# Optimization experiments

Measured on AMD Instinct MI355X. Metric: run time of the kernel, lower is better.

## Reference

```python
import jax, jax.numpy as jnp
import numpy as np

EMB = 256
N_NODES = 100000
N_EDGES = 500000
N_REL = 10
REL_DIM = 64
HID = 128
HEADS = 4
HEAD_DIM = HID // HEADS


def setup_inputs() -> dict:
    key = jax.random.key(0)
    ks = jax.random.split(key, 16)
    s = lambda i, shape: jax.random.normal(ks[i], shape, dtype=jnp.float32) * 0.05
    return {
        "node_embeddings": jax.random.normal(ks[0], (N_NODES, EMB), dtype=jnp.float32),
        "edge_index": jax.random.randint(ks[1], (2, N_EDGES), 0, N_NODES),
        "relation_type": jax.random.randint(ks[2], (N_EDGES,), 0, N_REL),
        "rel_emb": s(3, (N_REL, REL_DIM)),
        "W_edge": s(4, (2 * EMB, HID)), "b_edge": jnp.zeros((HID,), jnp.float32),
        "W_q": s(5, (REL_DIM, HID)), "b_q": jnp.zeros((HID,), jnp.float32),
        "W_k": s(6, (HID, HID)), "b_k": jnp.zeros((HID,), jnp.float32),
        "W_v": s(7, (HID, HID)), "b_v": jnp.zeros((HID,), jnp.float32),
        "W_o1": s(8, (HID, HID)), "b_o1": jnp.zeros((HID,), jnp.float32),
        "W_o2": s(9, (HID, 1)), "b_o2": jnp.zeros((1,), jnp.float32),
    }


def reference(node_embeddings, edge_index, relation_type, rel_emb,
              W_edge, b_edge, W_q, b_q, W_k, b_k, W_v, b_v,
              W_o1, b_o1, W_o2, b_o2):
    # Gather endpoint features: [E, 2*EMB]
    src = node_embeddings[edge_index[0]]
    tgt = node_embeddings[edge_index[1]]
    edge_features = jnp.concatenate([src, tgt], axis=1)
    # Edge MLP (dropout is identity at eval): [E, HID]
    edge_hidden = jax.nn.relu(edge_features @ W_edge + b_edge)
    # Relation embedding lookup: [E, REL_DIM]
    rel = rel_emb[relation_type]
    E = edge_hidden.shape[0]
    Q = (rel @ W_q + b_q).reshape(E, HEADS, HEAD_DIM)
    K = (edge_hidden @ W_k + b_k).reshape(E, HEADS, HEAD_DIM)
    V = (edge_hidden @ W_v + b_v).reshape(E, HEADS, HEAD_DIM)
    scale = jnp.sqrt(jnp.float32(HEAD_DIM))
    scores = jnp.sum(Q * K, axis=-1) / scale          # [E, HEADS]
    attn = jax.nn.softmax(scores, axis=-1)            # softmax over heads
    attended = (attn[..., None] * V).reshape(E, HID)
    output = attended + edge_hidden
    # Output MLP: Linear->ReLU->Linear(1)
    h = jax.nn.relu(output @ W_o1 + b_o1)
    score = (h @ W_o2 + b_o2).squeeze(-1)             # [E]
    return score
```

## Files before the change

### kernel.cpp

```cpp
#include <hip/hip_runtime.h>

#define EMB   256
#define HID   128
#define RELD  64
#define NREL  10
#define TE    128

typedef __attribute__((ext_vector_type(8)))  short bf16x8;
typedef __attribute__((ext_vector_type(16))) float f32x16;

__device__ __forceinline__ float bf16_to_f32(unsigned short u) {
    union { unsigned int i; float f; } v;
    v.i = ((unsigned int)u) << 16;
    return v.f;
}

__device__ __forceinline__ unsigned short f32_to_bf16(float x) {
    union { unsigned int i; float f; } v;
    v.f = x;
    unsigned int b = v.i;
    unsigned int rounded = b + 0x7fffu + ((b >> 16) & 1u);
    return (unsigned short)(rounded >> 16);
}

template <bool F32>
__device__ __forceinline__ float ldx(const void* p, size_t i) {
    if (F32) return ((const float*)p)[i];
    return bf16_to_f32(((const unsigned short*)p)[i]);
}

__device__ __forceinline__ bool detect_f32(const void* nodeEmb) {
    const float* f = (const float*)nodeEmb;
    float x = f[(threadIdx.x & 63) * 997];
    bool sane = isfinite(x) && fabsf(x) < 1.0e6f;
    unsigned long long m = __ballot(sane);
    return __popcll(m) >= 48;
}

__device__ __forceinline__ void gload16(const void* g, void* l) {
    __builtin_amdgcn_global_load_lds(
        (const __attribute__((address_space(1))) unsigned int*)g,
        (__attribute__((address_space(3))) unsigned int*)l, 16, 0, 0);
}

template <bool F32>
__device__ void prep_body(int vb, const void* W_edge, const void* W_k,
                          const void* W_v, const void* W_o1, const void* rel_emb,
                          const void* W_q, const void* b_q,
                          unsigned short* WTe, unsigned short* WTk,
                          unsigned short* WTv, unsigned short* WTo1, float* Qtab)
{
    if (vb < 448) {
        int idx = vb * 256 + threadIdx.x;
        if (idx < 65536) {
            int kc = idx >> 12, e = idx & 4095;
            int g = e >> 3, j = e & 7;
            int col = g & 127, kg = g >> 7;
            int k = kc * 32 + kg * 8 + j;
            WTe[idx] = f32_to_bf16(ldx<F32>(W_edge, (size_t)k * HID + col));
        } else if (idx < 65536 + 16384) {
            int i = idx - 65536;
            int kc = i >> 12, e = i & 4095;
            int g = e >> 3, j = e & 7;
            int col = g & 127, kg = (g >> 7) & 3;
            int k = kc * 32 + kg * 8 + j;
            WTk[i] = f32_to_bf16(ldx<F32>(W_k, (size_t)k * HID + col));
        } else if (idx < 65536 + 2 * 16384) {
            int i = idx - 65536 - 16384;
            int kc = i >> 12, e = i & 4095;
            int g = e >> 3, j = e & 7;
            int col = g & 127, kg = (g >> 7) & 3;
            int k = kc * 32 + kg * 8 + j;
            WTv[i] = f32_to_bf16(ldx<F32>(W_v, (size_t)k * HID + col));
        } else {
            int i = idx - 65536 - 2 * 16384;
            int kc = i >> 12, e = i & 4095;
            int g = e >> 3, j = e & 7;
            int col = g & 127, kg = (g >> 7) & 3;
            int k = kc * 32 + kg * 8 + j;
            WTo1[i] = f32_to_bf16(ldx<F32>(W_o1, (size_t)k * HID + col));
        }
    } else {
        const int t = threadIdx.x;
        const int c = t & (HID - 1);
        const int h = t >> 7;
        for (int r = h; r < NREL; r += 2) {
            float acc = 0.f;
            for (int d = 0; d < RELD; ++d)
                acc += ldx<F32>(rel_emb, r * RELD + d) * ldx<F32>(W_q, (size_t)d * HID + c);
            Qtab[r * HID + c] = acc + ldx<F32>(b_q, c);
        }
    }
}

__global__ void prep_kernel(const void* nodeEmb,
                            const void* W_edge, const void* W_k, const void* W_v,
                            const void* W_o1, const void* rel_emb, const void* W_q,
                            const void* b_q,
                            unsigned short* WTe, unsigned short* WTk,
                            unsigned short* WTv, unsigned short* WTo1, float* Qtab,
                            unsigned short* nodeBf16, int convBlocks,
                            unsigned long long nodeElems)
{
    bool f32 = detect_f32(nodeEmb);
    int b = blockIdx.x;
    if (b < convBlocks) {
        if (!f32) return;
        unsigned long long i = (unsigned long long)b * 2048ull + threadIdx.x * 8;
        if (i + 8 <= nodeElems) {
            const float* src = (const float*)nodeEmb + i;
            float4 f0 = *(const float4*)src;
            float4 f1 = *(const float4*)(src + 4);
            union { unsigned short us[8]; uint4 v; } pk;
            pk.us[0] = f32_to_bf16(f0.x); pk.us[1] = f32_to_bf16(f0.y);
            pk.us[2] = f32_to_bf16(f0.z); pk.us[3] = f32_to_bf16(f0.w);
            pk.us[4] = f32_to_bf16(f1.x); pk.us[5] = f32_to_bf16(f1.y);
            pk.us[6] = f32_to_bf16(f1.z); pk.us[7] = f32_to_bf16(f1.w);
            *(uint4*)(nodeBf16 + i) = pk.v;
        }
        return;
    }
    b -= convBlocks;
    if (f32) prep_body<true >(b, W_edge, W_k, W_v, W_o1, rel_emb, W_q, b_q,
                              WTe, WTk, WTv, WTo1, Qtab);
    else     prep_body<false>(b, W_edge, W_k, W_v, W_o1, rel_emb, W_q, b_q,
                              WTe, WTk, WTv, WTo1, Qtab);
}

struct __align__(16) Smem {
    unsigned short sHid[16 * 128 * 8];
    unsigned short SA[2][4096];
    unsigned short SB[2][4096];
    float sQf[NREL * HID];
    float sBias[5 * HID];
    float sSc[TE][4];
    float sAttn[TE][4];
    float sPart[TE][2];
    int   sSrc[TE], sTgt[TE], sRel[TE];
};

__device__ __forceinline__ int shid_idx(int row, int k) {
    return (((k >> 3) * 128 + row) << 3) + (k & 7);
}

template <bool F32, bool GBF16>
__device__ void fused_body(
    Smem& sm,
    const void* gsrc, const int* edgeIdx, const int* relType,
    const unsigned short* WTe, const unsigned short* WTk,
    const unsigned short* WTv, const unsigned short* WTo1,
    const void* b_edge, const void* b_k, const void* b_v,
    const void* b_o1, const void* W_o2, const void* b_o2,
    const float* Qtab, void* outp, int E)
{
    const int t   = threadIdx.x;
    const int l   = t & 63;
    const int w   = t >> 6;
    const int c   = l & 31;
    const int h5  = l >> 5;
    const int rt  = w >> 1;
    const int cg2 = w & 1;
    const int bs  = blockIdx.x * TE;
    const int aRow = 32 * rt + c;

    if (t < TE) {
        int e = bs + t;
        if (e >= E) e = E - 1;
        if (e < 0)  e = 0;
        sm.sSrc[t] = edgeIdx[e];
        sm.sTgt[t] = edgeIdx[E + e];
        int r = relType[e];
        if (r < 0) r = 0;
        if (r >= NREL) r = NREL - 1;
        sm.sRel[t] = r;
    }
    for (int i = t; i < 5 * HID; i += 512) {
        int which = i >> 7, j = i & (HID - 1);
        float v = (which == 0) ? ldx<F32>(b_edge, j)
                : (which == 1) ? ldx<F32>(b_k, j)
                : (which == 2) ? ldx<F32>(b_v, j)
                : (which == 3) ? ldx<F32>(b_o1, j)
                               : ldx<F32>(W_o2, j);
        sm.sBias[i] = v;
    }
    for (int i = t; i < NREL * HID; i += 512)
        sm.sQf[i] = Qtab[i];
    __syncthreads();

    const int    stS   = t >> 8;
    const int    stH5  = (t >> 7) & 1;
    const int    stRow = t & 127;
    const size_t rowOffS = (size_t)sm.sSrc[stRow] * EMB;
    const size_t rowOffT = (size_t)sm.sTgt[stRow] * EMB;
    const int    colSub  = stS * 16 + stH5 * 8;
    char* const  ldsWaveA0 = (char*)sm.SA[0] + w * 1024;
    char* const  ldsWaveA1 = (char*)sm.SA[1] + w * 1024;
    char* const  ldsWaveB0 = (char*)sm.SB[0] + w * 1024;
    char* const  ldsWaveB1 = (char*)sm.SB[1] + w * 1024;

    #define STAGE_A(kc, buf)                                                     \
    {                                                                            \
        size_t eoff = (((kc) < 8) ? rowOffS : rowOffT)                           \
                      + (size_t)(((kc) & 7) * 32 + colSub);                      \
        if (GBF16) {                                                             \
            gload16((const unsigned short*)gsrc + eoff,                          \
                    (buf) ? ldsWaveA1 : ldsWaveA0);                              \
        } else {                                                                 \
            const float* p_ = (const float*)gsrc + eoff;                         \
            float4 f0_ = *(const float4*)p_;                                     \
            float4 f1_ = *(const float4*)(p_ + 4);                               \
            union { unsigned short us[8]; uint4 v; } pk_;                        \
            pk_.us[0] = f32_to_bf16(f0_.x); pk_.us[1] = f32_to_bf16(f0_.y);      \
            pk_.us[2] = f32_to_bf16(f0_.z); pk_.us[3] = f32_to_bf16(f0_.w);      \
            pk_.us[4] = f32_to_bf16(f1_.x); pk_.us[5] = f32_to_bf16(f1_.y);      \
            pk_.us[6] = f32_to_bf16(f1_.z); pk_.us[7] = f32_to_bf16(f1_.w);      \
            *(uint4*)((char*)sm.SA[(buf)] + t * 16) = pk_.v;                     \
        }                                                                        \
    }

    #define STAGE_B(WT, kc, buf)                                                 \
        gload16((WT) + (kc) * 4096 + t * 8, (buf) ? ldsWaveB1 : ldsWaveB0);

    #define MFMA_SA(buf, accv)                                                   \
    {                                                                            \
        const char* sa_ = (const char*)sm.SA[(buf)];                             \
        const char* sb_ = (const char*)sm.SB[(buf)];                             \
        _Pragma("unroll")                                                        \
        for (int s_ = 0; s_ < 2; ++s_) {                                         \
            bf16x8 a_ = *(const bf16x8*)(sa_ + ((s_ * 256 + h5 * 128 + aRow) << 4)); \
            _Pragma("unroll")                                                    \
            for (int ct_ = 0; ct_ < 2; ++ct_) {                                  \
                bf16x8 b_ = *(const bf16x8*)                                     \
                    (sb_ + ((s_ * 256 + h5 * 128 + 64 * cg2 + 32 * ct_ + c) << 4)); \
                accv[ct_] = __builtin_amdgcn_mfma_f32_32x32x16_bf16(             \
                                a_, b_, accv[ct_], 0, 0, 0);                     \
            }                                                                    \
        }                                                                        \
    }

    #define MFMA_H(kc, buf, accv)                                                \
    {                                                                            \
        const char* sb_ = (const char*)sm.SB[(buf)];                             \
        _Pragma("unroll")                                                        \
        for (int s_ = 0; s_ < 2; ++s_) {                                         \
            bf16x8 a_ = *(const bf16x8*)((const char*)sm.sHid +                  \
                         ((((kc) * 4 + s_ * 2 + h5) * 128 + aRow) << 4));        \
            _Pragma("unroll")                                                    \
            for (int ct_ = 0; ct_ < 2; ++ct_) {                                  \
                bf16x8 b_ = *(const bf16x8*)                                     \
                    (sb_ + ((s_ * 256 + h5 * 128 + 64 * cg2 + 32 * ct_ + c) << 4)); \
                accv[ct_] = __builtin_amdgcn_mfma_f32_32x32x16_bf16(             \
                                a_, b_, accv[ct_], 0, 0, 0);                     \
            }                                                                    \
        }                                                                        \
    }

    f32x16 acc[2];
    acc[0] = (f32x16)(0.0f); acc[1] = (f32x16)(0.0f);
    STAGE_A(0, 0); STAGE_B(WTe, 0, 0);
    __syncthreads();
    #pragma unroll
    for (int kc = 0; kc < 16; ++kc) {
        int buf = kc & 1;
        if (kc < 15) { STAGE_A(kc + 1, buf ^ 1); STAGE_B(WTe, kc + 1, buf ^ 1); }
        MFMA_SA(buf, acc);
        __syncthreads();
    }
    {
        #pragma unroll
        for (int ct = 0; ct < 2; ++ct) {
            int col = 64 * cg2 + 32 * ct + c;
            float bb = sm.sBias[col];
            #pragma unroll
            for (int r = 0; r < 16; ++r) {
                int erow = 32 * rt + (r & 3) + 8 * (r >> 2) + 4 * h5;
                sm.sHid[shid_idx(erow, col)] = f32_to_bf16(fmaxf(acc[ct][r] + bb, 0.f));
            }
        }
    }

    f32x16 kacc[2];
    kacc[0] = (f32x16)(0.0f); kacc[1] = (f32x16)(0.0f);
    STAGE_B(WTk, 0, 0);
    __syncthreads();
    #pragma unroll
    for (int kc = 0; kc < 4; ++kc) {
        int buf = kc & 1;
        if (kc < 3) STAGE_B(WTk, kc + 1, buf ^ 1);
        MFMA_H(kc, buf, kacc);
        __syncthreads();
    }

    {
        float ps[2][16];
        #pragma unroll
        for (int ct = 0; ct < 2; ++ct) {
            int col = 64 * cg2 + 32 * ct + c;
            float bk = sm.sBias[HID + col];
            #pragma unroll
            for (int r = 0; r < 16; ++r) {
                int erow = 32 * rt + (r & 3) + 8 * (r >> 2) + 4 * h5;
                ps[ct][r] = (kacc[ct][r] + bk) * sm.sQf[sm.sRel[erow] * HID + col];
            }
        }
        #pragma unroll
        for (int m = 1; m < 32; m <<= 1)
            #pragma unroll
            for (int ct = 0; ct < 2; ++ct)
                #pragma unroll
                for (int r = 0; r < 16; ++r)
                    ps[ct][r] += __shfl_xor(ps[ct][r], m, 64);
        if (c == 0) {
            const float inv = 0.17677669529663687f;
            #pragma unroll
            for (int ct = 0; ct < 2; ++ct) {
                int head = 2 * cg2 + ct;
                #pragma unroll
                for (int r = 0; r < 16; ++r) {
                    int erow = 32 * rt + (r & 3) + 8 * (r >> 2) + 4 * h5;
                    sm.sSc[erow][head] = ps[ct][r] * inv;
                }
            }
        }
    }
    __syncthreads();
    if (t < TE) {
        float s0 = sm.sSc[t][0], s1 = sm.sSc[t][1];
        float s2 = sm.sSc[t][2], s3 = sm.sSc[t][3];
        float m = fmaxf(fmaxf(s0, s1), fmaxf(s2, s3));
        float e0 = expf(s0 - m), e1 = expf(s1 - m);
        float e2 = expf(s2 - m), e3 = expf(s3 - m);
        float den = e0 + e1 + e2 + e3;
        sm.sAttn[t][0] = e0 / den; sm.sAttn[t][1] = e1 / den;
        sm.sAttn[t][2] = e2 / den; sm.sAttn[t][3] = e3 / den;
    }
    __syncthreads();

    f32x16 vacc[2];
    vacc[0] = (f32x16)(0.0f); vacc[1] = (f32x16)(0.0f);
    STAGE_B(WTv, 0, 0);
    __syncthreads();
    #pragma unroll
    for (int kc = 0; kc < 4; ++kc) {
        int buf = kc & 1;
        if (kc < 3) STAGE_B(WTv, kc + 1, buf ^ 1);
        MFMA_H(kc, buf, vacc);
        __syncthreads();
    }

    {
        #pragma unroll
        for (int ct = 0; ct < 2; ++ct) {
            int col  = 64 * cg2 + 32 * ct + c;
            int head = 2 * cg2 + ct;
            float bv = sm.sBias[2 * HID + col];
            #pragma unroll
            for (int r = 0; r < 16; ++r) {
                int erow = 32 * rt + (r & 3) + 8 * (r >> 2) + 4 * h5;
                float at = sm.sAttn[erow][head];
                int   si = shid_idx(erow, col);
                float hv = bf16_to_f32(sm.sHid[si]);
                sm.sHid[si] = f32_to_bf16(at * (vacc[ct][r] + bv) + hv);
            }
        }
    }
    __syncthreads();

    f32x16 oacc[2];
    oacc[0] = (f32x16)(0.0f); oacc[1] = (f32x16)(0.0f);
    STAGE_B(WTo1, 0, 0);
    __syncthreads();
    #pragma unroll
    for (int kc = 0; kc < 4; ++kc) {
        int buf = kc & 1;
        if (kc < 3) STAGE_B(WTo1, kc + 1, buf ^ 1);
        MFMA_H(kc, buf, oacc);
        __syncthreads();
    }
    {
        float pr[16];
        #pragma unroll
        for (int r = 0; r < 16; ++r) pr[r] = 0.f;
        #pragma unroll
        for (int ct = 0; ct < 2; ++ct) {
            int col = 64 * cg2 + 32 * ct + c;
            float bo = sm.sBias[3 * HID + col];
            float wo = sm.sBias[4 * HID + col];
            #pragma unroll
            for (int r = 0; r < 16; ++r)
                pr[r] += fmaxf(oacc[ct][r] + bo, 0.f) * wo;
        }
        #pragma unroll
        for (int m = 1; m < 32; m <<= 1)
            #pragma unroll
            for (int r = 0; r < 16; ++r)
                pr[r] += __shfl_xor(pr[r], m, 64);
        if (c == 0) {
            #pragma unroll
            for (int r = 0; r < 16; ++r) {
                int erow = 32 * rt + (r & 3) + 8 * (r >> 2) + 4 * h5;
                sm.sPart[erow][cg2] = pr[r];
            }
        }
    }
    __syncthreads();
    if (t < TE) {
        int ge = bs + t;
        if (ge < E) {
            float val = sm.sPart[t][0] + sm.sPart[t][1] + ldx<F32>(b_o2, 0);
            if (F32) ((float*)outp)[ge] = val;
            else     ((unsigned short*)outp)[ge] = f32_to_bf16(val);
        }
    }

    #undef STAGE_A
    #undef STAGE_B
    #undef MFMA_SA
    #undef MFMA_H
}

__global__ __launch_bounds__(512, 4) void RelationAttentionMLPHead_10539849744626_kernel(
    const void* nodeEmb, const unsigned short* nodeBf16, int useConv,
    const int* edgeIdx, const int* relType,
    const unsigned short* WTe, const unsigned short* WTk,
    const unsigned short* WTv, const unsigned short* WTo1,
    const void* b_edge, const void* b_k, const void* b_v,
    const void* b_o1, const void* W_o2, const void* b_o2,
    const float* Qtab, void* outp, int E)
{
    __shared__ Smem sm;
    if (detect_f32(nodeEmb)) {
        if (useConv)
            fused_body<true, true >(sm, nodeBf16, edgeIdx, relType, WTe, WTk, WTv, WTo1,
                                    b_edge, b_k, b_v, b_o1, W_o2, b_o2, Qtab, outp, E);
        else
            fused_body<true, false>(sm, nodeEmb, edgeIdx, relType, WTe, WTk, WTv, WTo1,
                                    b_edge, b_k, b_v, b_o1, W_o2, b_o2, Qtab, outp, E);
    } else {
        fused_body<false, true>(sm, nodeEmb, edgeIdx, relType, WTe, WTk, WTv, WTo1,
                                b_edge, b_k, b_v, b_o1, W_o2, b_o2, Qtab, outp, E);
    }
}

extern "C" void kernel_launch(void* const* d_in, const int* in_sizes, int n_in,
                              void* d_out, int out_size, void* d_ws, size_t ws_size,
                              hipStream_t stream) {
    (void)n_in;

    const void* nodeEmb = d_in[0];
    const int*  edgeIdx = (const int*)d_in[1];
    const int*  relType = (const int*)d_in[2];
    const void* rel_emb = d_in[3];
    const void* W_edge  = d_in[4];
    const void* b_edge  = d_in[5];
    const void* W_q     = d_in[6];
    const void* b_q     = d_in[7];
    const void* W_k     = d_in[8];
    const void* b_k     = d_in[9];
    const void* W_v     = d_in[10];
    const void* b_v     = d_in[11];
    const void* W_o1    = d_in[12];
    const void* b_o1    = d_in[13];
    const void* W_o2    = d_in[14];
    const void* b_o2    = d_in[15];

    int E = out_size;
    if (E <= 0) E = in_sizes ? in_sizes[2] : 0;
    if (E <= 0) E = 500000;

    unsigned long long nodeElems =
        (in_sizes && in_sizes[0] > 0) ? (unsigned long long)in_sizes[0] : 25600000ull;

    char* ws = (char*)d_ws;
    float*          Qtab     = (float*)ws;
    unsigned short* WTe      = (unsigned short*)(ws + 8192);
    unsigned short* WTk      = (unsigned short*)(ws + 139264);
    unsigned short* WTv      = (unsigned short*)(ws + 172032);
    unsigned short* WTo1     = (unsigned short*)(ws + 204800);
    unsigned short* nodeBf16 = (unsigned short*)(ws + 237568);

    size_t need = 237568ull + nodeElems * 2ull;
    int useConv = (ws_size >= need) ? 1 : 0;
    int convBlocks = useConv ? (int)((nodeElems + 2047ull) / 2048ull) : 0;

    prep_kernel<<<convBlocks + 449, 256, 0, stream>>>(
        nodeEmb, W_edge, W_k, W_v, W_o1, rel_emb, W_q, b_q,
        WTe, WTk, WTv, WTo1, Qtab, nodeBf16, convBlocks, nodeElems);

    int grid = (E + TE - 1) / TE;
    if (grid < 1) grid = 1;

    RelationAttentionMLPHead_10539849744626_kernel<<<grid, 512, 0, stream>>>(
        nodeEmb, nodeBf16, useConv, edgeIdx, relType, WTe, WTk, WTv, WTo1,
        b_edge, b_k, b_v, b_o1, W_o2, b_o2, Qtab, d_out, E);
}
```

Baseline: 459.5 us.

## Bucket-sort edges by source node and remap blocks across XCDs for locality

Adds a three-kernel counting sort (histogram, scan, atomic scatter) that groups edges into 512 buckets by source node id. The fused kernel then processes edges in that permuted order and writes each output back to its original edge index. Block ids are also remapped so each of 8 chiplet groups gets a contiguous range of sorted work. The aim is better L2 reuse of source-node rows in the gather, paid for with three extra launches, atomic contention on the histogram, and scattered output writes; target-node gathers stay random.

```diff
diff --git a/kernel.cpp b/kernel.cpp
--- a/kernel.cpp
+++ b/kernel.cpp
@@ -5,6 +5,7 @@
 #define RELD  64
 #define NREL  10
 #define TE    128
+#define NB    512
 
 typedef __attribute__((ext_vector_type(8)))  short bf16x8;
 typedef __attribute__((ext_vector_type(16))) float f32x16;
@@ -48,7 +49,8 @@
                           const void* W_v, const void* W_o1, const void* rel_emb,
                           const void* W_q, const void* b_q,
                           unsigned short* WTe, unsigned short* WTk,
-                          unsigned short* WTv, unsigned short* WTo1, float* Qtab)
+                          unsigned short* WTv, unsigned short* WTo1, float* Qtab,
+                          int* hist)
 {
     if (vb < 448) {
         int idx = vb * 256 + threadIdx.x;
@@ -82,6 +84,7 @@
         }
     } else {
         const int t = threadIdx.x;
+        for (int i = t; i < 2 * NB; i += 256) hist[i] = 0;
         const int c = t & (HID - 1);
         const int h = t >> 7;
         for (int r = h; r < NREL; r += 2) {
@@ -100,7 +103,7 @@
                             unsigned short* WTe, unsigned short* WTk,
                             unsigned short* WTv, unsigned short* WTo1, float* Qtab,
                             unsigned short* nodeBf16, int convBlocks,
-                            unsigned long long nodeElems)
+                            unsigned long long nodeElems, int* hist)
 {
     bool f32 = detect_f32(nodeEmb);
     int b = blockIdx.x;
@@ -122,9 +125,46 @@
     }
     b -= convBlocks;
     if (f32) prep_body<true >(b, W_edge, W_k, W_v, W_o1, rel_emb, W_q, b_q,
-                              WTe, WTk, WTv, WTo1, Qtab);
+                              WTe, WTk, WTv, WTo1, Qtab, hist);
     else     prep_body<false>(b, W_edge, W_k, W_v, W_o1, rel_emb, W_q, b_q,
-                              WTe, WTk, WTv, WTo1, Qtab);
+                              WTe, WTk, WTv, WTo1, Qtab, hist);
+}
+
+__global__ void sort_hist_kernel(const int* edgeIdx, int E, int shift, int* hist) {
+    int e = blockIdx.x * 256 + threadIdx.x;
+    if (e < E) {
+        int b = edgeIdx[e] >> shift;
+        if (b < 0) b = 0;
+        if (b >= NB) b = NB - 1;
+        atomicAdd(&hist[b], 1);
+    }
+}
+
+__global__ void sort_scan_kernel(const int* hist, int* curs) {
+    __shared__ int tmp[NB];
+    int t = threadIdx.x;
+    int v0 = hist[t];
+    tmp[t] = v0;
+    __syncthreads();
+    for (int d = 1; d < NB; d <<= 1) {
+        int v = (t >= d) ? tmp[t - d] : 0;
+        __syncthreads();
+        tmp[t] += v;
+        __syncthreads();
+    }
+    curs[t] = tmp[t] - v0;
+}
+
+__global__ void sort_scatter_kernel(const int* edgeIdx, int E, int shift,
+                                    int* curs, int* perm) {
+    int e = blockIdx.x * 256 + threadIdx.x;
+    if (e < E) {
+        int b = edgeIdx[e] >> shift;
+        if (b < 0) b = 0;
+        if (b >= NB) b = NB - 1;
+        int pos = atomicAdd(&curs[b], 1);
+        perm[pos] = e;
+    }
 }
 
 struct __align__(16) Smem {
@@ -137,6 +177,7 @@
     float sAttn[TE][4];
     float sPart[TE][2];
     int   sSrc[TE], sTgt[TE], sRel[TE];
+    int   sEid[TE];
 };
 
 __device__ __forceinline__ int shid_idx(int row, int k) {
@@ -151,7 +192,7 @@
     const unsigned short* WTv, const unsigned short* WTo1,
     const void* b_edge, const void* b_k, const void* b_v,
     const void* b_o1, const void* W_o2, const void* b_o2,
-    const float* Qtab, void* outp, int E)
+    const float* Qtab, const int* perm, int usePerm, void* outp, int E)
 {
     const int t   = threadIdx.x;
     const int l   = t & 63;
@@ -160,13 +201,30 @@
     const int h5  = l >> 5;
     const int rt  = w >> 1;
     const int cg2 = w & 1;
-    const int bs  = blockIdx.x * TE;
+
+    int wi;
+    {
+        int G = (int)gridDim.x;
+        int b = (int)blockIdx.x;
+        if (usePerm) {
+            int q = G >> 3, r = G & 7;
+            int x = b & 7, o = b >> 3;
+            wi = (x < r) ? x * (q + 1) + o : r * (q + 1) + (x - r) * q + o;
+        } else {
+            wi = b;
+        }
+    }
+    const int bs   = wi * TE;
     const int aRow = 32 * rt + c;
 
     if (t < TE) {
-        int e = bs + t;
+        int ge = bs + t;
+        if (ge >= E) ge = E - 1;
+        if (ge < 0)  ge = 0;
+        int e = usePerm ? perm[ge] : ge;
+        if (e < 0)  e = 0;
         if (e >= E) e = E - 1;
-        if (e < 0)  e = 0;
+        sm.sEid[t] = e;
         sm.sSrc[t] = edgeIdx[e];
         sm.sTgt[t] = edgeIdx[E + e];
         int r = relType[e];
@@ -408,8 +466,9 @@
         int ge = bs + t;
         if (ge < E) {
             float val = sm.sPart[t][0] + sm.sPart[t][1] + ldx<F32>(b_o2, 0);
-            if (F32) ((float*)outp)[ge] = val;
-            else     ((unsigned short*)outp)[ge] = f32_to_bf16(val);
+            int oe = sm.sEid[t];
+            if (F32) ((float*)outp)[oe] = val;
+            else     ((unsigned short*)outp)[oe] = f32_to_bf16(val);
         }
     }
 
@@ -426,19 +485,22 @@
     const unsigned short* WTv, const unsigned short* WTo1,
     const void* b_edge, const void* b_k, const void* b_v,
     const void* b_o1, const void* W_o2, const void* b_o2,
-    const float* Qtab, void* outp, int E)
+    const float* Qtab, const int* perm, int usePerm, void* outp, int E)
 {
     __shared__ Smem sm;
     if (detect_f32(nodeEmb)) {
         if (useConv)
             fused_body<true, true >(sm, nodeBf16, edgeIdx, relType, WTe, WTk, WTv, WTo1,
-                                    b_edge, b_k, b_v, b_o1, W_o2, b_o2, Qtab, outp, E);
+                                    b_edge, b_k, b_v, b_o1, W_o2, b_o2, Qtab,
+                                    perm, usePerm, outp, E);
         else
             fused_body<true, false>(sm, nodeEmb, edgeIdx, relType, WTe, WTk, WTv, WTo1,
-                                    b_edge, b_k, b_v, b_o1, W_o2, b_o2, Qtab, outp, E);
+                                    b_edge, b_k, b_v, b_o1, W_o2, b_o2, Qtab,
+                                    perm, usePerm, outp, E);
     } else {
         fused_body<false, true>(sm, nodeEmb, edgeIdx, relType, WTe, WTk, WTv, WTo1,
-                                b_edge, b_k, b_v, b_o1, W_o2, b_o2, Qtab, outp, E);
+                                b_edge, b_k, b_v, b_o1, W_o2, b_o2, Qtab,
+                                perm, usePerm, outp, E);
     }
 }
 
@@ -470,27 +532,43 @@
 
     unsigned long long nodeElems =
         (in_sizes && in_sizes[0] > 0) ? (unsigned long long)in_sizes[0] : 25600000ull;
+    unsigned long long nodeRows = nodeElems / EMB;
+    if (nodeRows < 1) nodeRows = 1;
+
+    int shift = 0;
+    while (((nodeRows - 1ull) >> shift) >= (unsigned long long)NB) ++shift;
 
     char* ws = (char*)d_ws;
-    float*          Qtab     = (float*)ws;
-    unsigned short* WTe      = (unsigned short*)(ws + 8192);
-    unsigned short* WTk      = (unsigned short*)(ws + 139264);
-    unsigned short* WTv      = (unsigned short*)(ws + 172032);
-    unsigned short* WTo1     = (unsigned short*)(ws + 204800);
-    unsigned short* nodeBf16 = (unsigned short*)(ws + 237568);
-
-    size_t need = 237568ull + nodeElems * 2ull;
-    int useConv = (ws_size >= need) ? 1 : 0;
-    int convBlocks = useConv ? (int)((nodeElems + 2047ull) / 2048ull) : 0;
+    float*          Qtab = (float*)ws;
+    unsigned short* WTe  = (unsigned short*)(ws + 8192);
+    unsigned short* WTk  = (unsigned short*)(ws + 139264);
+    unsigned short* WTv  = (unsigned short*)(ws + 172032);
+    unsigned short* WTo1 = (unsigned short*)(ws + 204800);
+    int*            hist = (int*)(ws + 237568);
+    int*            curs = (int*)(ws + 239616);
+    int*            perm = (int*)(ws + 241664);
+    unsigned long long permBytes = ((unsigned long long)E * 4ull + 255ull) & ~255ull;
+    unsigned short* nodeBf16 = (unsigned short*)(ws + 241664 + permBytes);
+
+    size_t need = 241664ull + permBytes + nodeElems * 2ull;
+    int useAll = (ws_size >= need) ? 1 : 0;
+    int convBlocks = useAll ? (int)((nodeElems + 2047ull) / 2048ull) : 0;
 
     prep_kernel<<<convBlocks + 449, 256, 0, stream>>>(
         nodeEmb, W_edge, W_k, W_v, W_o1, rel_emb, W_q, b_q,
-        WTe, WTk, WTv, WTo1, Qtab, nodeBf16, convBlocks, nodeElems);
+        WTe, WTk, WTv, WTo1, Qtab, nodeBf16, convBlocks, nodeElems, hist);
+
+    if (useAll) {
+        int sgrid = (E + 255) / 256;
+        sort_hist_kernel<<<sgrid, 256, 0, stream>>>(edgeIdx, E, shift, hist);
+        sort_scan_kernel<<<1, NB, 0, stream>>>(hist, curs);
+        sort_scatter_kernel<<<sgrid, 256, 0, stream>>>(edgeIdx, E, shift, curs, perm);
+    }
 
     int grid = (E + TE - 1) / TE;
     if (grid < 1) grid = 1;
 
     RelationAttentionMLPHead_10539849744626_kernel<<<grid, 512, 0, stream>>>(
-        nodeEmb, nodeBf16, useConv, edgeIdx, relType, WTe, WTk, WTv, WTo1,
-        b_edge, b_k, b_v, b_o1, W_o2, b_o2, Qtab, d_out, E);
-}
+        nodeEmb, nodeBf16, useAll, edgeIdx, relType, WTe, WTk, WTv, WTo1,
+        b_edge, b_k, b_v, b_o1, W_o2, b_o2, Qtab, perm, useAll, d_out, E);
+}
```

After: 822.0 us. +78.9%, slower.

## Deepen LDS staging pipeline with explicit vmcnt waits and cross-stage weight prefetch

Applied to the files above, without the earlier changes.

Replaces __syncthreads-based double buffering with a two-ahead prefetch scheme. Explicit s_waitcnt vmcnt counts and raw s_barrier wrapped in sched_barrier let loads for later chunks stay in flight across the barrier. The first weight tiles of each following GEMM stage (W_k, W_v, W_o1) are issued before the current stage's epilogue, so weight loads overlap the epilogue math. The vmcnt counts assume a fixed number of outstanding loads per stage, which is fragile for the F32 path that converts through registers and may miscount. The inline-asm waits also limit compiler scheduling.

```diff
diff --git a/kernel.cpp b/kernel.cpp
--- a/kernel.cpp
+++ b/kernel.cpp
@@ -41,6 +41,18 @@
     __builtin_amdgcn_global_load_lds(
         (const __attribute__((address_space(1))) unsigned int*)g,
         (__attribute__((address_space(3))) unsigned int*)l, 16, 0, 0);
+}
+
+#define WAITVL(n) asm volatile("s_waitcnt vmcnt(" #n ") lgkmcnt(0)" ::: "memory")
+
+__device__ __forceinline__ void sbar() {
+    __builtin_amdgcn_sched_barrier(0);
+    __builtin_amdgcn_s_barrier();
+    __builtin_amdgcn_sched_barrier(0);
+}
+__device__ __forceinline__ void bar_lds() {
+    asm volatile("s_waitcnt lgkmcnt(0)" ::: "memory");
+    sbar();
 }
 
 template <bool F32>
@@ -187,12 +199,10 @@
         sm.sQf[i] = Qtab[i];
     __syncthreads();
 
-    const int    stS   = t >> 8;
-    const int    stH5  = (t >> 7) & 1;
     const int    stRow = t & 127;
     const size_t rowOffS = (size_t)sm.sSrc[stRow] * EMB;
     const size_t rowOffT = (size_t)sm.sTgt[stRow] * EMB;
-    const int    colSub  = stS * 16 + stH5 * 8;
+    const int    colSub  = (t >> 8) * 16 + ((t >> 7) & 1) * 8;
     char* const  ldsWaveA0 = (char*)sm.SA[0] + w * 1024;
     char* const  ldsWaveA1 = (char*)sm.SA[1] + w * 1024;
     char* const  ldsWaveB0 = (char*)sm.SB[0] + w * 1024;
@@ -258,14 +268,17 @@
     f32x16 acc[2];
     acc[0] = (f32x16)(0.0f); acc[1] = (f32x16)(0.0f);
     STAGE_A(0, 0); STAGE_B(WTe, 0, 0);
-    __syncthreads();
+    STAGE_A(1, 1); STAGE_B(WTe, 1, 1);
     #pragma unroll
     for (int kc = 0; kc < 16; ++kc) {
         int buf = kc & 1;
-        if (kc < 15) { STAGE_A(kc + 1, buf ^ 1); STAGE_B(WTe, kc + 1, buf ^ 1); }
+        if (kc < 15) { WAITVL(2); } else { WAITVL(0); }
+        sbar();
         MFMA_SA(buf, acc);
-        __syncthreads();
-    }
+        sbar();
+        if (kc < 14) { STAGE_A(kc + 2, buf); STAGE_B(WTe, kc + 2, buf); }
+    }
+    STAGE_B(WTk, 0, 0); STAGE_B(WTk, 1, 1);
     {
         #pragma unroll
         for (int ct = 0; ct < 2; ++ct) {
@@ -278,18 +291,20 @@
             }
         }
     }
+    bar_lds();
 
     f32x16 kacc[2];
     kacc[0] = (f32x16)(0.0f); kacc[1] = (f32x16)(0.0f);
-    STAGE_B(WTk, 0, 0);
-    __syncthreads();
     #pragma unroll
     for (int kc = 0; kc < 4; ++kc) {
         int buf = kc & 1;
-        if (kc < 3) STAGE_B(WTk, kc + 1, buf ^ 1);
+        if (kc < 3) { WAITVL(1); } else { WAITVL(0); }
+        sbar();
         MFMA_H(kc, buf, kacc);
-        __syncthreads();
-    }
+        sbar();
+        if (kc < 2) STAGE_B(WTk, kc + 2, buf);
+    }
+    STAGE_B(WTv, 0, 0); STAGE_B(WTv, 1, 1);
 
     {
         float ps[2][16];
@@ -323,7 +338,7 @@
             }
         }
     }
-    __syncthreads();
+    bar_lds();
     if (t < TE) {
         float s0 = sm.sSc[t][0], s1 = sm.sSc[t][1];
         float s2 = sm.sSc[t][2], s3 = sm.sSc[t][3];
@@ -334,19 +349,20 @@
         sm.sAttn[t][0] = e0 / den; sm.sAttn[t][1] = e1 / den;
         sm.sAttn[t][2] = e2 / den; sm.sAttn[t][3] = e3 / den;
     }
-    __syncthreads();
+    bar_lds();
 
     f32x16 vacc[2];
     vacc[0] = (f32x16)(0.0f); vacc[1] = (f32x16)(0.0f);
-    STAGE_B(WTv, 0, 0);
-    __syncthreads();
     #pragma unroll
     for (int kc = 0; kc < 4; ++kc) {
         int buf = kc & 1;
-        if (kc < 3) STAGE_B(WTv, kc + 1, buf ^ 1);
+        if (kc < 3) { WAITVL(1); } else { WAITVL(0); }
+        sbar();
         MFMA_H(kc, buf, vacc);
-        __syncthreads();
-    }
+        sbar();
+        if (kc < 2) STAGE_B(WTv, kc + 2, buf);
+    }
+    STAGE_B(WTo1, 0, 0); STAGE_B(WTo1, 1, 1);
 
     {
         #pragma unroll
@@ -364,18 +380,18 @@
             }
         }
     }
-    __syncthreads();
+    bar_lds();
 
     f32x16 oacc[2];
     oacc[0] = (f32x16)(0.0f); oacc[1] = (f32x16)(0.0f);
-    STAGE_B(WTo1, 0, 0);
-    __syncthreads();
     #pragma unroll
     for (int kc = 0; kc < 4; ++kc) {
         int buf = kc & 1;
-        if (kc < 3) STAGE_B(WTo1, kc + 1, buf ^ 1);
+        if (kc < 3) { WAITVL(1); } else { WAITVL(0); }
+        sbar();
         MFMA_H(kc, buf, oacc);
-        __syncthreads();
+        sbar();
+        if (kc < 2) STAGE_B(WTo1, kc + 2, buf);
     }
     {
         float pr[16];
@@ -403,7 +419,7 @@
             }
         }
     }
-    __syncthreads();
+    bar_lds();
     if (t < TE) {
         int ge = bs + t;
         if (ge < E) {
```

New measurement: 435.0 us. -5.3%, faster.
